# Kernel optimization log

Measured on AMD Instinct MI355X. Metric: run time of the kernel, lower is better.

Reference implementation:

```python
import jax, jax.numpy as jnp
import numpy as np
from jax import lax

B, T, H, W, C = 1, 8, 32, 32, 512


def _rmsnorm(x, gamma):
    # x / (||x||_2 + 1e-8) * sqrt(C) * gamma  (matches FlaxHunyuanVideo15RMSNorm)
    n = x / (jnp.linalg.norm(x, axis=-1, keepdims=True) + 1e-8)
    return n * (x.shape[-1] ** 0.5) * gamma


def _conv3d(x, w, b):
    # x: [B,T,H,W,Cin], w: [kt,kh,kw,Cin,Cout] (DHWIO), VALID padding
    y = lax.conv_general_dilated(x, w, (1, 1, 1), 'VALID',
                                 dimension_numbers=('NDHWC', 'DHWIO', 'NDHWC'))
    return y + b


def _causal_conv3d(x, w, b):
    # replicate pad: time (2,0) causal, spatial (1,1) each side, then valid 3x3x3 conv
    xp = jnp.pad(x, [(0, 0), (2, 0), (1, 1), (1, 1), (0, 0)], mode='edge')
    return _conv3d(xp, w, b)


def _conv1x1(x, w, b):
    # w: [1,1,1,Cin,Cout]
    return jnp.einsum('bthwc,cd->bthwd', x, w[0, 0, 0]) + b


def _resnet(x, g1, w1, b1, g2, w2, b2):
    h = jax.nn.silu(_rmsnorm(x, g1))
    h = _causal_conv3d(h, w1, b1)
    h = jax.nn.silu(_rmsnorm(h, g2))
    h = _causal_conv3d(h, w2, b2)
    return h + x


def _attn(x, g, qw, qb, kw, kb, vw, vb, pw, pb):
    identity = x
    xn = _rmsnorm(x, g)
    b, t, h, w, c = xn.shape
    n_hw = h * w
    s = t * n_hw
    q = _conv1x1(xn, qw, qb).reshape(b, s, c)
    k = _conv1x1(xn, kw, kb).reshape(b, s, c)
    v = _conv1x1(xn, vw, vb).reshape(b, s, c)
    # block-causal frame mask: query at frame f attends to keys with frame <= f
    fid = jnp.arange(s) // n_hw
    mask = jnp.where(fid[None, :] <= fid[:, None], 0.0, -jnp.inf).astype(q.dtype)
    scale = 1.0 / jnp.sqrt(jnp.asarray(c, q.dtype))
    scores = jnp.einsum('bqc,bkc->bqk', q, k) * scale + mask  # [B,S,S]
    attn = jax.nn.softmax(scores, axis=-1)
    o = jnp.einsum('bqk,bkc->bqc', attn, v).reshape(b, t, h, w, c)
    o = _conv1x1(o, pw, pb)
    return o + identity


def _forward(x, r1_g1, r1_w1, r1_b1, r1_g2, r1_w2, r1_b2,
             at_g, q_w, q_b, k_w, k_b, v_w, v_b, p_w, p_b,
             r2_g1, r2_w1, r2_b1, r2_g2, r2_w2, r2_b2):
    h = _resnet(x, r1_g1, r1_w1, r1_b1, r1_g2, r1_w2, r1_b2)
    h = _attn(h, at_g, q_w, q_b, k_w, k_b, v_w, v_b, p_w, p_b)
    h = _resnet(h, r2_g1, r2_w1, r2_b1, r2_g2, r2_w2, r2_b2)
    return h


def setup_inputs() -> dict:
    key = jax.random.key(0)
    ks = jax.random.split(key, 10)
    w3 = lambda k: jax.random.normal(k, (3, 3, 3, C, C), jnp.float32) * 0.02
    w1 = lambda k: jax.random.normal(k, (1, 1, 1, C, C), jnp.float32) * 0.02
    zc = jnp.zeros((C,), jnp.float32)
    oc = jnp.ones((C,), jnp.float32)
    return dict(
        x=jax.random.normal(ks[0], (B, T, H, W, C), jnp.float32),
        r1_g1=oc, r1_w1=w3(ks[1]), r1_b1=zc,
        r1_g2=oc, r1_w2=w3(ks[2]), r1_b2=zc,
        at_g=oc,
        q_w=w1(ks[3]), q_b=zc,
        k_w=w1(ks[4]), k_b=zc,
        v_w=w1(ks[5]), v_b=zc,
        p_w=w1(ks[6]), p_b=zc,
        r2_g1=oc, r2_w1=w3(ks[7]), r2_b1=zc,
        r2_g2=oc, r2_w2=w3(ks[8]), r2_b2=zc,
    )


def reference(x, r1_g1, r1_w1, r1_b1, r1_g2, r1_w2, r1_b2,
              at_g, q_w, q_b, k_w, k_b, v_w, v_b, p_w, p_b,
              r2_g1, r2_w1, r2_b1, r2_g2, r2_w2, r2_b2):
    return _forward(x, r1_g1, r1_w1, r1_b1, r1_g2, r1_w2, r1_b2,
                    at_g, q_w, q_b, k_w, k_b, v_w, v_b, p_w, p_b,
                    r2_g1, r2_w1, r2_b1, r2_g2, r2_w2, r2_b2)
```

## Files before the change

### kernel.cpp

```cpp
#include <hip/hip_runtime.h>
#include <cstdint>
#include <cstddef>

typedef __attribute__((ext_vector_type(4))) float floatx4;
typedef __attribute__((ext_vector_type(8))) short short8;

__device__ __forceinline__ short f2bf(float x) {
  union { float f; unsigned u; } c; c.f = x;
  unsigned r = (c.u + 0x7FFFu + ((c.u >> 16) & 1u)) >> 16;
  return (short)r;
}

__device__ __forceinline__ float bf2f(short x) {
  union { unsigned u; float f; } c; c.u = ((unsigned)(unsigned short)x) << 16;
  return c.f;
}

__device__ __forceinline__ floatx4 mfma16(short8 a, short8 b, floatx4 c) {
  return __builtin_amdgcn_mfma_f32_16x16x32_bf16(a, b, c, 0, 0, 0);
}

template <typename T>
__device__ __forceinline__ void gl_lds16(const T* g, T* l) {
  __builtin_amdgcn_global_load_lds(
      (__attribute__((address_space(1))) void*)g,
      (__attribute__((address_space(3))) void*)l, 16, 0, 0);
}

template <bool PAD, bool SILU>
__global__ __launch_bounds__(256) void norm_kernel(const float* __restrict__ src,
                                                   const float* __restrict__ gamma,
                                                   short* __restrict__ dst) {
  const int tid = threadIdx.x;
  const int wv = tid >> 6, lane = tid & 63;
  const int id = blockIdx.x * 4 + wv;
  int srow;
  if (PAD) {
    int tp = id / 1156, rem = id - tp * 1156;
    int hp = rem / 34, wp = rem - hp * 34;
    int t = tp - 2; t = t < 0 ? 0 : t;
    int h = hp - 1; h = h < 0 ? 0 : (h > 31 ? 31 : h);
    int w = wp - 1; w = w < 0 ? 0 : (w > 31 ? 31 : w);
    srow = (t << 10) + (h << 5) + w;
  } else {
    srow = id;
  }
  const float* sp = src + (size_t)srow * 512 + lane * 8;
  float4 v0 = *(const float4*)sp;
  float4 v1 = *(const float4*)(sp + 4);
  float a[8] = {v0.x, v0.y, v0.z, v0.w, v1.x, v1.y, v1.z, v1.w};
  float ss = 0.f;
#pragma unroll
  for (int i = 0; i < 8; ++i) ss += a[i] * a[i];
#pragma unroll
  for (int off = 32; off > 0; off >>= 1) ss += __shfl_xor(ss, off);
  const float scale = 22.627416997969522f / (sqrtf(ss) + 1e-8f);
  const float* gp = gamma + lane * 8;
  float4 g0 = *(const float4*)gp;
  float4 g1 = *(const float4*)(gp + 4);
  float g[8] = {g0.x, g0.y, g0.z, g0.w, g1.x, g1.y, g1.z, g1.w};
  short8 ov;
#pragma unroll
  for (int i = 0; i < 8; ++i) {
    float y = a[i] * scale * g[i];
    if (SILU) y = y / (1.f + __expf(-y));
    ov[i] = f2bf(y);
  }
  *(short8*)(dst + (size_t)id * 512 + lane * 8) = ov;
}

template <int NP>
__global__ __launch_bounds__(256) void combine_norm(const float* __restrict__ P0,
                                                    const float* __restrict__ P1,
                                                    const float* __restrict__ P2,
                                                    const float* __restrict__ bias,
                                                    const float* __restrict__ gamma,
                                                    short* __restrict__ dst) {
  const int tid = threadIdx.x;
  const int wv = tid >> 6, lane = tid & 63;
  const int id = blockIdx.x * 4 + wv;
  int tp = id / 1156, rem = id - tp * 1156;
  int hp = rem / 34, wp = rem - hp * 34;
  int t = tp - 2; t = t < 0 ? 0 : t;
  int h = hp - 1; h = h < 0 ? 0 : (h > 31 ? 31 : h);
  int w = wp - 1; w = w < 0 ? 0 : (w > 31 ? 31 : w);
  const size_t base = (size_t)((t << 10) + (h << 5) + w) * 512 + lane * 8;
  float a[8];
  {
    float4 a0 = *(const float4*)(P0 + base), a1 = *(const float4*)(P0 + base + 4);
    float4 b0 = *(const float4*)(P1 + base), b1 = *(const float4*)(P1 + base + 4);
    float4 z0 = *(const float4*)(bias + lane * 8), z1 = *(const float4*)(bias + lane * 8 + 4);
    a[0] = a0.x + b0.x + z0.x; a[1] = a0.y + b0.y + z0.y;
    a[2] = a0.z + b0.z + z0.z; a[3] = a0.w + b0.w + z0.w;
    a[4] = a1.x + b1.x + z1.x; a[5] = a1.y + b1.y + z1.y;
    a[6] = a1.z + b1.z + z1.z; a[7] = a1.w + b1.w + z1.w;
    if (NP == 3) {
      float4 c0 = *(const float4*)(P2 + base), c1 = *(const float4*)(P2 + base + 4);
      a[0] += c0.x; a[1] += c0.y; a[2] += c0.z; a[3] += c0.w;
      a[4] += c1.x; a[5] += c1.y; a[6] += c1.z; a[7] += c1.w;
    }
  }
  float ss = 0.f;
#pragma unroll
  for (int i = 0; i < 8; ++i) ss += a[i] * a[i];
#pragma unroll
  for (int off = 32; off > 0; off >>= 1) ss += __shfl_xor(ss, off);
  const float scale = 22.627416997969522f / (sqrtf(ss) + 1e-8f);
  float4 g0 = *(const float4*)(gamma + lane * 8), g1 = *(const float4*)(gamma + lane * 8 + 4);
  float g[8] = {g0.x, g0.y, g0.z, g0.w, g1.x, g1.y, g1.z, g1.w};
  short8 ov;
#pragma unroll
  for (int i = 0; i < 8; ++i) {
    float y = a[i] * scale * g[i];
    y = y / (1.f + __expf(-y));
    ov[i] = f2bf(y);
  }
  *(short8*)(dst + (size_t)id * 512 + lane * 8) = ov;
}

__global__ __launch_bounds__(256) void transpose_w(const float* __restrict__ src,
                                                   short* __restrict__ dst, int R, int C) {
  __shared__ float t[32][33];
  const int tx = threadIdx.x & 31, ty = threadIdx.x >> 5;
  const int r0 = (int)blockIdx.x << 5, c0 = (int)blockIdx.y << 5;
#pragma unroll
  for (int i = 0; i < 4; ++i)
    t[ty + i * 8][tx] = src[(size_t)(r0 + ty + i * 8) * C + c0 + tx];
  __syncthreads();
#pragma unroll
  for (int i = 0; i < 4; ++i)
    dst[(size_t)(c0 + ty + i * 8) * R + r0 + tx] = f2bf(t[tx][ty + i * 8]);
}

template <int NP>
__global__ __launch_bounds__(256) void conv_gemm_sp(const short* __restrict__ Xp,
                                                    const short* __restrict__ WT,
                                                    float* __restrict__ P0,
                                                    float* __restrict__ P1,
                                                    float* __restrict__ P2) {
  __shared__ __attribute__((aligned(16))) short Alds[2][4096];
  __shared__ __attribute__((aligned(16))) short Blds[2][4096];
  const int tid = threadIdx.x;
  const int wv = tid >> 6, lane = tid & 63;
  const int m0 = (int)blockIdx.x << 7, n0 = (int)blockIdx.y << 7;
  const int z = blockIdx.z;
  float* __restrict__ dst = (NP == 3) ? (z == 0 ? P0 : (z == 1 ? P1 : P2))
                                      : (z ? P1 : P0);

  int aoff[2], boff[2];
#pragma unroll
  for (int j = 0; j < 2; ++j) {
    const int chunk = wv * 2 + j;
    const int m = m0 + chunk * 16 + (lane >> 2);
    const int t = m >> 10, h = (m >> 5) & 31, w = m & 31;
    aoff[j] = (t * 1156 + h * 34 + w) * 512 + (lane & 3) * 8;
    const int n = n0 + chunk * 16 + (lane >> 2);
    boff[j] = n * 13824 + (lane & 3) * 8;
  }
  const int wm = (wv & 1) << 6, wn = (wv >> 1) << 6;
  floatx4 acc[4][4];
#pragma unroll
  for (int i = 0; i < 4; ++i)
#pragma unroll
    for (int j = 0; j < 4; ++j) acc[i][j] = 0.f;

  const int la = (lane & 15) * 32 + (lane >> 4) * 8;
  const int span = 432 / NP;
  const int k0 = z * span, k1 = k0 + span;

  auto stage = [&](int kk, int buf) {
    const int tap = kk >> 4;
    const int cin0 = (kk & 15) << 5;
    const int dt = tap / 9;
    const int r9 = tap - dt * 9;
    const int dh = r9 / 3;
    const int dw = r9 - dh * 3;
    const int tapoff = (dt * 1156 + dh * 34 + dw) * 512 + cin0;
#pragma unroll
    for (int j = 0; j < 2; ++j) {
      const int chunk = wv * 2 + j;
      gl_lds16(Xp + aoff[j] + tapoff, &Alds[buf][chunk * 512]);
      gl_lds16(WT + boff[j] + (kk << 5), &Blds[buf][chunk * 512]);
    }
  };

  stage(k0, 0);
  for (int kk = k0; kk < k1; ++kk) {
    const int cur = (kk - k0) & 1;
    __syncthreads();
    if (kk + 1 < k1) stage(kk + 1, cur ^ 1);
    short8 af[4], bf[4];
#pragma unroll
    for (int i = 0; i < 4; ++i) af[i] = *(const short8*)&Alds[cur][(wm + i * 16) * 32 + la];
#pragma unroll
    for (int j = 0; j < 4; ++j) bf[j] = *(const short8*)&Blds[cur][(wn + j * 16) * 32 + la];
#pragma unroll
    for (int i = 0; i < 4; ++i)
#pragma unroll
      for (int j = 0; j < 4; ++j) acc[i][j] = mfma16(af[i], bf[j], acc[i][j]);
  }

  const int rbase = m0 + wm + (lane >> 4) * 4;
#pragma unroll
  for (int i = 0; i < 4; ++i) {
    const int row = rbase + i * 16;
#pragma unroll
    for (int j = 0; j < 4; ++j) {
      const int col = n0 + wn + j * 16 + (lane & 15);
#pragma unroll
      for (int r = 0; r < 4; ++r)
        dst[(size_t)(row + r) * 512 + col] = acc[i][j][r];
    }
  }
}

template <int NP, bool HAS_RES>
__global__ __launch_bounds__(256) void conv_combine(const float* __restrict__ P0,
                                                    const float* __restrict__ P1,
                                                    const float* __restrict__ P2,
                                                    const float* __restrict__ bias,
                                                    const float* __restrict__ res,
                                                    float* __restrict__ out) {
  const size_t i = ((size_t)blockIdx.x * 256 + threadIdx.x) * 4;
  float4 a = *(const float4*)(P0 + i);
  float4 b = *(const float4*)(P1 + i);
  float4 bz = *(const float4*)(bias + (int)(i & 511));
  float4 r;
  r.x = a.x + b.x + bz.x;
  r.y = a.y + b.y + bz.y;
  r.z = a.z + b.z + bz.z;
  r.w = a.w + b.w + bz.w;
  if (NP == 3) {
    float4 c = *(const float4*)(P2 + i);
    r.x += c.x; r.y += c.y; r.z += c.z; r.w += c.w;
  }
  if (HAS_RES) {
    float4 rs = *(const float4*)(res + i);
    r.x += rs.x; r.y += rs.y; r.z += rs.z; r.w += rs.w;
  }
  *(float4*)(out + i) = r;
}

template <int EPI>
__global__ __launch_bounds__(256) void gemm_bt(const short* __restrict__ A,
                                               const short* __restrict__ BT, int kdim,
                                               const float* __restrict__ b0,
                                               const float* __restrict__ b1,
                                               const float* __restrict__ b2,
                                               short* __restrict__ o0,
                                               short* __restrict__ o1,
                                               short* __restrict__ o2,
                                               float* oF, const float* res) {
  __shared__ __attribute__((aligned(16))) short Alds[2][4096];
  __shared__ __attribute__((aligned(16))) short Blds[2][4096];
  const int tid = threadIdx.x;
  const int wv = tid >> 6, lane = tid & 63;
  const int m0 = (int)blockIdx.x << 7, n0 = (int)blockIdx.y << 7;
  int aoff[2], boff[2];
#pragma unroll
  for (int j = 0; j < 2; ++j) {
    const int chunk = wv * 2 + j;
    aoff[j] = (m0 + chunk * 16 + (lane >> 2)) * kdim + (lane & 3) * 8;
    boff[j] = (n0 + chunk * 16 + (lane >> 2)) * kdim + (lane & 3) * 8;
  }
  const int wm = (wv & 1) << 6, wn = (wv >> 1) << 6;
  floatx4 acc[4][4];
#pragma unroll
  for (int i = 0; i < 4; ++i)
#pragma unroll
    for (int j = 0; j < 4; ++j) acc[i][j] = 0.f;
  const int la = (lane & 15) * 32 + (lane >> 4) * 8;
  const int kiters = kdim >> 5;

  auto stage = [&](int kk, int buf) {
#pragma unroll
    for (int j = 0; j < 2; ++j) {
      const int chunk = wv * 2 + j;
      gl_lds16(A + aoff[j] + (kk << 5), &Alds[buf][chunk * 512]);
      gl_lds16(BT + boff[j] + (kk << 5), &Blds[buf][chunk * 512]);
    }
  };

  stage(0, 0);
  for (int kk = 0; kk < kiters; ++kk) {
    const int cur = kk & 1;
    __syncthreads();
    if (kk + 1 < kiters) stage(kk + 1, cur ^ 1);
    short8 af[4], bf[4];
#pragma unroll
    for (int i = 0; i < 4; ++i) af[i] = *(const short8*)&Alds[cur][(wm + i * 16) * 32 + la];
#pragma unroll
    for (int j = 0; j < 4; ++j) bf[j] = *(const short8*)&Blds[cur][(wn + j * 16) * 32 + la];
#pragma unroll
    for (int i = 0; i < 4; ++i)
#pragma unroll
      for (int j = 0; j < 4; ++j) acc[i][j] = mfma16(af[i], bf[j], acc[i][j]);
  }

  const int rbase = m0 + wm + (lane >> 4) * 4;
#pragma unroll
  for (int i = 0; i < 4; ++i) {
    const int row = rbase + i * 16;
#pragma unroll
    for (int j = 0; j < 4; ++j) {
      const int col = n0 + wn + j * 16 + (lane & 15);
      if (EPI == 0) {
        const int sel = col >> 9;
        const int c = col & 511;
        const float* bp = sel == 0 ? b0 : (sel == 1 ? b1 : b2);
        const float bz = bp[c];
#pragma unroll
        for (int r = 0; r < 4; ++r) {
          const int rr = row + r;
          const short v = f2bf(acc[i][j][r] + bz);
          if (sel == 0) {
            o0[(size_t)rr * 512 + c] = v;
          } else if (sel == 1) {
            o1[(size_t)(rr >> 5) * 16384 + ((c >> 5) << 10) + (((c >> 3) & 3) << 8) +
               ((rr & 31) << 3) + (c & 7)] = v;
          } else {
            o2[(size_t)(rr >> 5) * 16384 + (((rr >> 3) & 3) << 12) + (c << 3) + (rr & 7)] = v;
          }
        }
      } else {
        const float bz = b0[col];
#pragma unroll
        for (int r = 0; r < 4; ++r) {
          const size_t idx = (size_t)(row + r) * 512 + col;
          oF[idx] = acc[i][j][r] + bz + res[idx];
        }
      }
    }
  }
}

__global__ __launch_bounds__(256, 2) void attn_partial(const short* __restrict__ Q,
                                                       const short* __restrict__ Ksw,
                                                       const short* __restrict__ Vsw,
                                                       short* __restrict__ OpA,
                                                       short* __restrict__ OpB,
                                                       float* __restrict__ Lp) {
  __shared__ __attribute__((aligned(16))) short Klds[16384];
  __shared__ __attribute__((aligned(16))) short Vlds[16384];
  __shared__ __attribute__((aligned(16))) short Plds[4][512];
  const int tid = threadIdx.x;
  const int wv = tid >> 6, lane = tid & 63;
  const int cl = lane & 15, quad = lane >> 4;
  const int bid = (int)blockIdx.x;
  const int x8 = bid & 7, jj = bid >> 3;
  int y, qb;
  if (jj < 64) {
    y = x8 + ((jj >> 4) << 3);
    qb = jj & 15;
  } else {
    const int L = x8 * 8 + (jj - 64);
    y = 32 + (L >> 4);
    qb = L & 15;
  }
  int f = 0;
  while ((f + 1) * (f + 2) / 2 <= y) ++f;
  const int chunk = y - f * (f + 1) / 2;
  const int pidx = y * 16 + qb;
  const int q0 = (f << 10) + (qb << 6);

  short8 qf[16];
  {
    const short* qp = Q + (size_t)(q0 + wv * 16 + cl) * 512 + quad * 8;
#pragma unroll
    for (int kc = 0; kc < 16; ++kc) qf[kc] = *(const short8*)(qp + kc * 32);
  }
  floatx4 o[32];
#pragma unroll
  for (int i = 0; i < 32; ++i) o[i] = 0.f;
  float lr[4] = {0.f, 0.f, 0.f, 0.f};
  const float c1 = 0.063758716f;
  const short* klb = Klds + quad * 256 + cl * 8;
  const short* vlb = Vlds + quad * 4096 + cl * 8;
  const int swr = ((cl >> 1) & 3) << 3;

  for (int kt = 0; kt < 32; ++kt) {
    const size_t tb = (size_t)((chunk << 5) + kt) * 16384;
#pragma unroll
    for (int j = 0; j < 8; ++j) {
      const int row = (j * 4 + wv) << 9;
      gl_lds16(Ksw + tb + row + lane * 8, &Klds[row]);
      gl_lds16(Vsw + tb + row + lane * 8, &Vlds[row]);
    }
    __syncthreads();

    floatx4 s0 = 0.f, s1 = 0.f;
#pragma unroll
    for (int kc = 0; kc < 16; ++kc) {
      short8 k0 = *(const short8*)(klb + kc * 1024);
      short8 k1 = *(const short8*)(klb + kc * 1024 + 128);
      s0 = mfma16(qf[kc], k0, s0);
      s1 = mfma16(qf[kc], k1, s1);
    }

#pragma unroll
    for (int r = 0; r < 4; ++r) {
      const float p0 = exp2f(s0[r] * c1), p1 = exp2f(s1[r] * c1);
      lr[r] += p0 + p1;
      const int qlr = quad * 4 + r;
      const int sw = ((qlr >> 1) & 3) << 3;
      const int oi = qlr * 32 + (cl ^ sw);
      Plds[wv][oi] = f2bf(p0);
      Plds[wv][oi ^ 16] = f2bf(p1);
    }
    const short8 pf = *(const short8*)&Plds[wv][cl * 32 + ((quad << 3) ^ swr)];
#pragma unroll
    for (int cn = 0; cn < 32; ++cn) {
      const short8 vf = *(const short8*)(vlb + cn * 128);
      o[cn] = mfma16(pf, vf, o[cn]);
    }
    __syncthreads();
  }

#pragma unroll
  for (int r = 0; r < 4; ++r) {
    float v = lr[r];
    v += __shfl_xor(v, 1);
    v += __shfl_xor(v, 2);
    v += __shfl_xor(v, 4);
    v += __shfl_xor(v, 8);
    lr[r] = v;
  }

  short* base = pidx < 216 ? OpA + (size_t)pidx * 32768 : OpB + (size_t)(pidx - 216) * 32768;
  const int lrow0 = wv * 16 + quad * 4;
#pragma unroll
  for (int cn = 0; cn < 32; ++cn) {
    const int col = cn * 16 + cl;
#pragma unroll
    for (int r = 0; r < 4; ++r)
      base[(size_t)(lrow0 + r) * 512 + col] = f2bf(o[cn][r]);
  }
  if (cl == 0) {
#pragma unroll
    for (int r = 0; r < 4; ++r) Lp[pidx * 64 + lrow0 + r] = lr[r];
  }
}

__global__ __launch_bounds__(256) void attn_combine(const short* __restrict__ OpA,
                                                    const short* __restrict__ OpB,
                                                    const float* __restrict__ Lp,
                                                    short* __restrict__ O) {
  const int tid = threadIdx.x;
  const int wv = tid >> 6, lane = tid & 63;
  const int row = (int)blockIdx.x * 4 + wv;
  const int f = row >> 10, n = f + 1;
  const int qb = (row >> 6) & 15, lrow = row & 63;
  const int tri = f * (f + 1) / 2;
  float den = 0.f, acc[8];
#pragma unroll
  for (int i = 0; i < 8; ++i) acc[i] = 0.f;
#pragma unroll
  for (int ch = 0; ch < 8; ++ch) {
    if (ch < n) {
      const int pidx = (tri + ch) * 16 + qb;
      den += Lp[pidx * 64 + lrow];
      const short* b = pidx < 216 ? OpA + (size_t)pidx * 32768 : OpB + (size_t)(pidx - 216) * 32768;
      const short8 v = *(const short8*)(b + (size_t)lrow * 512 + lane * 8);
#pragma unroll
      for (int i = 0; i < 8; ++i) acc[i] += bf2f(v[i]);
    }
  }
  const float inv = 1.f / den;
  short8 ov;
#pragma unroll
  for (int i = 0; i < 8; ++i) ov[i] = f2bf(acc[i] * inv);
  *(short8*)(O + (size_t)row * 512 + lane * 8) = ov;
}

extern "C" void kernel_launch(void* const* d_in, const int* in_sizes, int n_in,
                              void* d_out, int out_size, void* d_ws, size_t ws_size,
                              hipStream_t stream) {
  const float* x     = (const float*)d_in[0];
  const float* r1_g1 = (const float*)d_in[1];
  const float* r1_w1 = (const float*)d_in[2];
  const float* r1_b1 = (const float*)d_in[3];
  const float* r1_g2 = (const float*)d_in[4];
  const float* r1_w2 = (const float*)d_in[5];
  const float* r1_b2 = (const float*)d_in[6];
  const float* at_g  = (const float*)d_in[7];
  const float* q_w   = (const float*)d_in[8];
  const float* q_b   = (const float*)d_in[9];
  const float* k_w   = (const float*)d_in[10];
  const float* k_b   = (const float*)d_in[11];
  const float* v_w   = (const float*)d_in[12];
  const float* v_b   = (const float*)d_in[13];
  const float* p_w   = (const float*)d_in[14];
  const float* p_b   = (const float*)d_in[15];
  const float* r2_g1 = (const float*)d_in[16];
  const float* r2_w1 = (const float*)d_in[17];
  const float* r2_b1 = (const float*)d_in[18];
  const float* r2_g2 = (const float*)d_in[19];
  const float* r2_w2 = (const float*)d_in[20];
  const float* r2_b2 = (const float*)d_in[21];
  float* out = (float*)d_out;

  char* ws = (char*)d_ws;
  size_t off = 0;
  auto alloc = [&](size_t bytes) -> void* {
    void* p = ws + off;
    off = (off + bytes + 255) & ~(size_t)255;
    return p;
  };
  short* wT    = (short*)alloc(27ull * 512 * 512 * 2);
  short* wqkvT = (short*)alloc(1536ull * 512 * 2);
  short* pwT   = (short*)alloc(512ull * 512 * 2);
  short* Xp    = (short*)alloc(10ull * 34 * 34 * 512 * 2);
  float* Y     = (float*)alloc(8192ull * 512 * 4);
  float* hA    = (float*)alloc(8192ull * 512 * 4);
  short* xn    = (short*)alloc(8192ull * 512 * 2);
  short* Qb    = (short*)alloc(8192ull * 512 * 2);
  short* Ksw   = (short*)alloc(8192ull * 512 * 2);
  short* Vsw   = (short*)alloc(8192ull * 512 * 2);
  float* Lp    = (float*)alloc(576ull * 64 * 4);
  (void)ws_size; (void)in_sizes; (void)n_in; (void)out_size;

  short* OpA = wT;
  short* OpB = Xp;
  float* P0  = (float*)xn;
  float* P1  = (float*)Ksw;
  float* P2  = Y;

  const dim3 b256(256);
  const dim3 convg3(64, 4, 3);
  const dim3 convg2(64, 4, 2);

  transpose_w<<<dim3(432, 16), b256, 0, stream>>>(r1_w1, wT, 13824, 512);
  norm_kernel<true, true><<<2890, b256, 0, stream>>>(x, r1_g1, Xp);
  conv_gemm_sp<3><<<convg3, b256, 0, stream>>>(Xp, wT, P0, P1, P2);
  transpose_w<<<dim3(432, 16), b256, 0, stream>>>(r1_w2, wT, 13824, 512);
  combine_norm<3><<<2890, b256, 0, stream>>>(P0, P1, P2, r1_b1, r1_g2, Xp);
  conv_gemm_sp<3><<<convg3, b256, 0, stream>>>(Xp, wT, P0, P1, P2);
  conv_combine<3, true><<<4096, b256, 0, stream>>>(P0, P1, P2, r1_b2, x, hA);

  norm_kernel<false, false><<<2048, b256, 0, stream>>>(hA, at_g, xn);
  transpose_w<<<dim3(16, 16), b256, 0, stream>>>(q_w, wqkvT, 512, 512);
  transpose_w<<<dim3(16, 16), b256, 0, stream>>>(k_w, wqkvT + 512 * 512, 512, 512);
  transpose_w<<<dim3(16, 16), b256, 0, stream>>>(v_w, wqkvT + 1024 * 512, 512, 512);
  transpose_w<<<dim3(16, 16), b256, 0, stream>>>(p_w, pwT, 512, 512);
  gemm_bt<0><<<dim3(64, 12), b256, 0, stream>>>(xn, wqkvT, 512, q_b, k_b, v_b,
                                                Qb, Ksw, Vsw, nullptr, nullptr);
  attn_partial<<<576, b256, 0, stream>>>(Qb, Ksw, Vsw, OpA, OpB, Lp);
  attn_combine<<<2048, b256, 0, stream>>>(OpA, OpB, Lp, xn);
  gemm_bt<1><<<dim3(64, 4), b256, 0, stream>>>(xn, pwT, 512, p_b, nullptr, nullptr,
                                               nullptr, nullptr, nullptr, hA, hA);

  transpose_w<<<dim3(432, 16), b256, 0, stream>>>(r2_w1, wT, 13824, 512);
  norm_kernel<true, true><<<2890, b256, 0, stream>>>(hA, r2_g1, Xp);
  conv_gemm_sp<2><<<convg2, b256, 0, stream>>>(Xp, wT, P0, P1, P2);
  transpose_w<<<dim3(432, 16), b256, 0, stream>>>(r2_w2, wT, 13824, 512);
  combine_norm<2><<<2890, b256, 0, stream>>>(P0, P1, P2, r2_b1, r2_g2, Xp);
  conv_gemm_sp<2><<<convg2, b256, 0, stream>>>(Xp, wT, P0, P1, P2);
  conv_combine<2, true><<<4096, b256, 0, stream>>>(P0, P1, P2, r2_b2, hA, out);
}
```

Baseline: 1.069 ms.

## Split K/V staging in attention loop to overlap loads with MFMA

Splits the per-tile K and V LDS staging so the next tile's K load is issued right after QK^T and the next V load right after PV, with partial vmcnt waits and raw barriers in place of full syncthreads. This lets global-to-LDS transfers overlap the softmax and MFMA phases instead of stalling at the start of each iteration. It also raises wave priority around the MFMA blocks. The risks are correctness in the hand-counted waitcnt and barrier placement, plus extra barriers per iteration.

New measurement: 1.049 ms. Within noise of the previous version (-1.8%).

```diff
diff --git a/kernel.cpp b/kernel.cpp
--- a/kernel.cpp
+++ b/kernel.cpp
@@ -26,6 +26,9 @@
       (__attribute__((address_space(1))) void*)g,
       (__attribute__((address_space(3))) void*)l, 16, 0, 0);
 }
+
+#define MEMFENCE asm volatile("" ::: "memory")
+#define WAITV8 asm volatile("s_waitcnt vmcnt(8)" ::: "memory")
 
 template <bool PAD, bool SILU>
 __global__ __launch_bounds__(256) void norm_kernel(const float* __restrict__ src,
@@ -378,17 +381,33 @@
   const short* vlb = Vlds + quad * 4096 + cl * 8;
   const int swr = ((cl >> 1) & 3) << 3;
 
-  for (int kt = 0; kt < 32; ++kt) {
+  auto stageK = [&](int kt) {
     const size_t tb = (size_t)((chunk << 5) + kt) * 16384;
 #pragma unroll
     for (int j = 0; j < 8; ++j) {
       const int row = (j * 4 + wv) << 9;
       gl_lds16(Ksw + tb + row + lane * 8, &Klds[row]);
+    }
+  };
+  auto stageV = [&](int kt) {
+    const size_t tb = (size_t)((chunk << 5) + kt) * 16384;
+#pragma unroll
+    for (int j = 0; j < 8; ++j) {
+      const int row = (j * 4 + wv) << 9;
       gl_lds16(Vsw + tb + row + lane * 8, &Vlds[row]);
     }
-    __syncthreads();
+  };
+
+  stageK(0);
+  stageV(0);
+
+  for (int kt = 0; kt < 32; ++kt) {
+    WAITV8;
+    __builtin_amdgcn_s_barrier();
+    MEMFENCE;
 
     floatx4 s0 = 0.f, s1 = 0.f;
+    __builtin_amdgcn_s_setprio(1);
 #pragma unroll
     for (int kc = 0; kc < 16; ++kc) {
       short8 k0 = *(const short8*)(klb + kc * 1024);
@@ -396,6 +415,12 @@
       s0 = mfma16(qf[kc], k0, s0);
       s1 = mfma16(qf[kc], k1, s1);
     }
+    __builtin_amdgcn_s_setprio(0);
+
+    MEMFENCE;
+    __builtin_amdgcn_s_barrier();
+    MEMFENCE;
+    if (kt + 1 < 32) stageK(kt + 1);
 
 #pragma unroll
     for (int r = 0; r < 4; ++r) {
@@ -407,13 +432,24 @@
       Plds[wv][oi] = f2bf(p0);
       Plds[wv][oi ^ 16] = f2bf(p1);
     }
+
+    WAITV8;
+    __builtin_amdgcn_s_barrier();
+    MEMFENCE;
+
     const short8 pf = *(const short8*)&Plds[wv][cl * 32 + ((quad << 3) ^ swr)];
+    __builtin_amdgcn_s_setprio(1);
 #pragma unroll
     for (int cn = 0; cn < 32; ++cn) {
       const short8 vf = *(const short8*)(vlb + cn * 128);
       o[cn] = mfma16(pf, vf, o[cn]);
     }
-    __syncthreads();
+    __builtin_amdgcn_s_setprio(0);
+
+    MEMFENCE;
+    __builtin_amdgcn_s_barrier();
+    MEMFENCE;
+    if (kt + 1 < 32) stageV(kt + 1);
   }
 
 #pragma unroll
```
